# Performance work log

Measured on AMD Instinct MI355X. Metric: run time of the kernel, lower is better.

The kernel has to match this reference:

```python
import jax, jax.numpy as jnp
import numpy as np

EPS = 1e-6
INPUT_SIZE = 64
NUM_LEAVES = INPUT_SIZE
NUM_LAYERS = NUM_LEAVES - 1
BATCH = 262144
SINKHORN_ITERS = 20


def _clip01(v):
    return jnp.clip(v, EPS, 1.0 - EPS)


def _F_base(x, y, a, w0, w1):
    # Branches of F for a in [0.5, 2] (the non-recursive region), selected branchlessly.
    x = _clip01(x)
    y = _clip01(y)
    lin = w0 * x + w1 * y
    p = jnp.sqrt(3.0 / jnp.maximum(2.0 - a, EPS)) - 1.0
    g = (x ** (2.0 * w0) * y ** (2.0 * w1)) ** p
    rule0 = jnp.where((jnp.abs(x - 1.0) < EPS) & (jnp.abs(y - 1.0) < EPS), 1.0, 0.0)
    return jnp.where(
        jnp.abs(a - 2.0) < EPS, rule0,
        jnp.where(a >= 0.75, g,
                  jnp.where(a > 0.5, (3.0 - 4.0 * a) * lin + (4.0 * a - 2.0) * g, lin)))


def _F(x, y, a, w0, w1):
    # Full generalized_gcd F with the single-level De Morgan reflection for a < 0.5.
    x = _clip01(x)
    y = _clip01(y)
    hi = _F_base(x, y, a, w0, w1)
    a_ref = jnp.clip(1.0 - a, -1.0 + EPS, 2.0 - EPS)
    lo = 1.0 - _F_base(1.0 - x, 1.0 - y, a_ref, w0, w1)
    lin = w0 * x + w1 * y
    return jnp.where(jnp.abs(a - 0.5) < EPS, lin, jnp.where(a < 0.5, lo, hi))


def _sinkhorn(logits, n_iter=SINKHORN_ITERS):
    # Log-space Sinkhorn normalization -> (approximately) doubly-stochastic P.
    l = logits
    for _ in range(n_iter):
        l = l - jax.nn.logsumexp(l, axis=1, keepdims=True)
        l = l - jax.nn.logsumexp(l, axis=0, keepdims=True)
    return jnp.exp(l)


def setup_inputs() -> dict:
    key = jax.random.key(0)
    k1, k2, k3, k4 = jax.random.split(key, 4)
    x = jax.random.uniform(k1, (BATCH, INPUT_SIZE), dtype=jnp.float32)
    logits = jax.random.normal(k2, (INPUT_SIZE, NUM_LEAVES), dtype=jnp.float32)
    weights = jax.random.uniform(k3, (NUM_LAYERS,), dtype=jnp.float32)
    biases = jax.random.uniform(k4, (NUM_LAYERS,), dtype=jnp.float32)
    return {"x": x, "logits": logits, "weights": weights, "biases": biases}


def reference(x, logits, weights, biases):
    P = _sinkhorn(logits)                 # [INPUT_SIZE, NUM_LEAVES], columns sum to 1
    leaves = (x @ P).T                    # [NUM_LEAVES, BATCH]

    def step(carry, inp):
        leaf, w, b = inp
        nres = _F(carry, leaf, b, w, 1.0 - w)
        nres = jnp.where(jnp.isnan(nres), b, nres)  # NaN fallback to bias, as in torch forward
        return nres, None

    # Left-leaning tree: state_0 = leaf_0; state_i = F(state_{i-1}, leaf_i, b, w, 1-w)
    final, _ = jax.lax.scan(step, leaves[0], (leaves[1:], weights, biases))
    return final[:, None]                 # [BATCH, 1]
```

## Files before the change

kernel.cpp:

```cpp
#include <hip/hip_runtime.h>
#include <hip/hip_bf16.h>
#include <math.h>

#define EPS 1e-6f
#define N 64
#define NLAYERS 63
#define SINK_ITERS 20
#define LOG2E 1.4426950408889634f

typedef __attribute__((ext_vector_type(8))) short bf16x8;
typedef __attribute__((ext_vector_type(4))) float f32x4;

__device__ __forceinline__ float fast_log2(float v) {
#if __has_builtin(__builtin_amdgcn_logf)
  return __builtin_amdgcn_logf(v);
#else
  return log2f(v);
#endif
}
__device__ __forceinline__ float fast_exp2(float v) {
#if __has_builtin(__builtin_amdgcn_exp2f)
  return __builtin_amdgcn_exp2f(v);
#else
  return exp2f(v);
#endif
}

__device__ __forceinline__ unsigned short f2bf(float f) {
  unsigned int u = __float_as_uint(f);
  return (unsigned short)((u + 0x7FFFu + ((u >> 16) & 1u)) >> 16);
}

__device__ __forceinline__ bf16x8 pack8(float4 a, float4 b) {
  union { unsigned short us[8]; bf16x8 v; } u;
  u.us[0] = f2bf(a.x); u.us[1] = f2bf(a.y);
  u.us[2] = f2bf(a.z); u.us[3] = f2bf(a.w);
  u.us[4] = f2bf(b.x); u.us[5] = f2bf(b.y);
  u.us[6] = f2bf(b.z); u.us[7] = f2bf(b.w);
  return u.v;
}

__global__ __launch_bounds__(64) void sinkhorn_kernel(
    const float* __restrict__ logits,
    const float* __restrict__ weights,
    const float* __restrict__ biases,
    unsigned short* __restrict__ Pfrag,
    float* __restrict__ layers) {
  __shared__ float T[64 * 65 + 128];
  const int l = threadIdx.x;

  float K[64];
  {
    const float4* lr = (const float4*)(logits + (l << 6));
    #pragma unroll
    for (int q = 0; q < 16; ++q) {
      float4 t = lr[q];
      K[4*q+0] = fast_exp2(t.x * LOG2E);
      K[4*q+1] = fast_exp2(t.y * LOG2E);
      K[4*q+2] = fast_exp2(t.z * LOG2E);
      K[4*q+3] = fast_exp2(t.w * LOG2E);
    }
  }
  #pragma unroll
  for (int j = 0; j < 64; ++j) T[l * 65 + j] = K[j];
  __syncthreads();
  float KT[64];
  #pragma unroll
  for (int k = 0; k < 64; ++k) KT[k] = T[k * 65 + l];
  __syncthreads();

  float* Uv = &T[64 * 65];
  float* Vv = &T[64 * 65 + 64];
  const float4* Uv4 = (const float4*)Uv;
  const float4* Vv4 = (const float4*)Vv;
  Vv[l] = 1.0f;
  __syncthreads();

  float u = 1.0f;
  for (int it = 0; it < SINK_ITERS; ++it) {
    float s0 = 0.f, s1 = 0.f, s2 = 0.f, s3 = 0.f;
    #pragma unroll
    for (int q = 0; q < 16; ++q) {
      float4 v = Vv4[q];
      s0 = fmaf(K[4*q+0], v.x, s0);
      s1 = fmaf(K[4*q+1], v.y, s1);
      s2 = fmaf(K[4*q+2], v.z, s2);
      s3 = fmaf(K[4*q+3], v.w, s3);
    }
    u = 1.0f / ((s0 + s1) + (s2 + s3));
    __syncthreads();
    Uv[l] = u;
    __syncthreads();
    float c0 = 0.f, c1 = 0.f, c2 = 0.f, c3 = 0.f;
    #pragma unroll
    for (int q = 0; q < 16; ++q) {
      float4 uu = Uv4[q];
      c0 = fmaf(KT[4*q+0], uu.x, c0);
      c1 = fmaf(KT[4*q+1], uu.y, c1);
      c2 = fmaf(KT[4*q+2], uu.z, c2);
      c3 = fmaf(KT[4*q+3], uu.w, c3);
    }
    float v = 1.0f / ((c0 + c1) + (c2 + c3));
    __syncthreads();
    Vv[l] = v;
    __syncthreads();
  }

  #pragma unroll
  for (int j = 0; j < 64; ++j) T[l * 65 + j] = u * K[j] * Vv[j];
  __syncthreads();

  #pragma unroll
  for (int s = 0; s < 2; ++s)
    #pragma unroll
    for (int t = 0; t < 4; ++t) {
      union { unsigned short us[8]; bf16x8 v; } buf;
      #pragma unroll
      for (int j = 0; j < 8; ++j)
        buf.us[j] = f2bf(T[(s*32 + ((l >> 4) << 3) + j) * 65 + t*16 + (l & 15)]);
      *(bf16x8*)(Pfrag + (((s*4 + t) * 64 + l) << 3)) = buf.v;
    }

  if (l < NLAYERS) {
    float w0 = weights[l];
    float w1 = 1.0f - w0;
    float a  = biases[l];
    float e0, e1, cl, cg, sgn;
    if (fabsf(a - 0.5f) < EPS) {
      e0 = 0.f; e1 = 0.f; cl = 1.f; cg = 0.f; sgn = 1.f;
    } else {
      float ae;
      if (a < 0.5f) { sgn = -1.f; ae = fminf(fmaxf(1.0f - a, -1.0f + EPS), 2.0f - EPS); }
      else          { sgn =  1.f; ae = a; }
      float pp = sqrtf(3.0f / fmaxf(2.0f - ae, EPS)) - 1.0f;
      if (ae >= 0.75f) { cl = 0.0f;            cg = 1.0f; }
      else             { cl = 3.0f - 4.0f*ae;  cg = 4.0f*ae - 2.0f; }
      e0 = 2.0f * w0 * pp;
      e1 = 2.0f * w1 * pp;
    }
    float* Lr = layers + l * 8;
    Lr[0] = w0; Lr[1] = w1; Lr[2] = e0; Lr[3] = e1;
    Lr[4] = cl; Lr[5] = cg; Lr[6] = a;  Lr[7] = sgn;
  }
}

__global__ __launch_bounds__(256, 2) void scan_kernel(
    const float* __restrict__ x,
    const unsigned short* __restrict__ Pfrag,
    const float* __restrict__ layers,
    float* __restrict__ out) {
  __shared__ float Lv[256 * 36];
  const int tid = threadIdx.x;
  const int w = tid >> 6, l = tid & 63;
  const int q = l >> 4, c = l & 15;
  const size_t rowbase = (size_t)blockIdx.x << 8;
  const float4* Lp4 = (const float4*)layers;

  bf16x8 Bf[2][4];
  #pragma unroll
  for (int s = 0; s < 2; ++s)
    #pragma unroll
    for (int t = 0; t < 4; ++t)
      Bf[s][t] = *(const bf16x8*)(Pfrag + (((s*4 + t) * 64 + l) << 3));

  bf16x8 Af[4][2];
  #pragma unroll
  for (int i = 0; i < 4; ++i) {
    const float* rp = x + (rowbase + (w << 6) + (i << 4) + c) * 64 + (q << 3);
    float4 a0 = *(const float4*)(rp);
    float4 a1 = *(const float4*)(rp + 4);
    float4 b0 = *(const float4*)(rp + 32);
    float4 b1 = *(const float4*)(rp + 36);
    Af[i][0] = pack8(a0, a1);
    Af[i][1] = pack8(b0, b1);
  }

  float st = 0.f;
  #pragma unroll
  for (int half = 0; half < 2; ++half) {
    #pragma unroll
    for (int rt = 0; rt < 4; ++rt) {
      #pragma unroll
      for (int lt = 0; lt < 2; ++lt) {
        f32x4 acc = {0.f, 0.f, 0.f, 0.f};
        acc = __builtin_amdgcn_mfma_f32_16x16x32_bf16(Bf[0][(half<<1)+lt], Af[rt][0], acc, 0, 0, 0);
        acc = __builtin_amdgcn_mfma_f32_16x16x32_bf16(Bf[1][(half<<1)+lt], Af[rt][1], acc, 0, 0, 0);
        const int row  = (w << 6) + (rt << 4) + c;
        const int nloc = (lt << 4) + (q << 2);
        *(f32x4*)&Lv[row * 36 + nloc] = acc;
      }
    }
    f32x4 Lf[8];
    #pragma unroll
    for (int i = 0; i < 8; ++i)
      Lf[i] = *(f32x4*)&Lv[tid * 36 + (i << 2)];

    const int j0 = (half == 0) ? 1 : 32;
    const int nst = (half == 0) ? 31 : 32;

    float ylin[32], ylog[32];
    #pragma unroll
    for (int k = 0; k < 32; ++k) {
      if (k < nst) {
        const int j = j0 + k;
        const int jl = j - (half << 5);
        float4 p0 = Lp4[(j - 1) * 2];
        float4 p1 = Lp4[(j - 1) * 2 + 1];
        const float sgn = p1.w;
        const float off = fmaf(-0.5f, sgn, 0.5f);
        float yy = fminf(fmaxf(Lf[jl >> 2][jl & 3], EPS), 1.0f - EPS);
        float yr = fmaf(sgn, yy, off);
        ylin[k] = p0.y * yr;
        ylog[k] = p0.w * fast_log2(yr);
      }
    }

    if (half == 0) st = Lf[0][0];
    #pragma unroll
    for (int k = 0; k < 32; ++k) {
      if (k < nst) {
        const int j = j0 + k;
        float4 p0 = Lp4[(j - 1) * 2];
        float4 p1 = Lp4[(j - 1) * 2 + 1];
        const float sgn = p1.w;
        const float off = fmaf(-0.5f, sgn, 0.5f);
        float xx = fminf(fmaxf(st, EPS), 1.0f - EPS);
        xx = fmaf(sgn, xx, off);
        float lin = fmaf(p0.x, xx, ylin[k]);
        float g   = fast_exp2(fmaf(p0.z, fast_log2(xx), ylog[k]));
        float r   = fmaf(p1.x, lin, p1.y * g);
        st = fmaf(sgn, r, off);
      }
    }
  }

  out[rowbase + tid] = st;
}

extern "C" void kernel_launch(void* const* d_in, const int* in_sizes, int n_in,
                              void* d_out, int out_size, void* d_ws, size_t ws_size,
                              hipStream_t stream) {
  const float* x       = (const float*)d_in[0];
  const float* logits  = (const float*)d_in[1];
  const float* weights = (const float*)d_in[2];
  const float* biases  = (const float*)d_in[3];
  float* out = (float*)d_out;

  unsigned short* Pfrag = (unsigned short*)d_ws;
  float* layers = (float*)((char*)d_ws + 8 * 64 * 8 * sizeof(unsigned short));

  const int batch = out_size;

  hipLaunchKernelGGL(sinkhorn_kernel, dim3(1), dim3(64), 0, stream,
                     logits, weights, biases, Pfrag, layers);
  hipLaunchKernelGGL(scan_kernel, dim3(batch / 256), dim3(256), 0, stream,
                     x, Pfrag, layers, out);
}
```

Measured before the change: 120.5 us.

## Fold reflection signs and coefficients into layer table, chunk scan for occupancy

Precomputes per-layer combined reflection sign/offset, pre-multiplied linear weights and a log2 of the g coefficient, so each scan step uses fewer ops and the state stays in reflected space between layers. The scan is split into 8-layer chunks with a non-unrolled loop to cut register use, and launch bounds rise from 2 to 4 blocks per SM. The bf16 conversion now uses the packed hardware convert instruction, and x loads are issued before the fragment loads. Risks include changed rounding (hardware convert vs manual round-to-nearest-even), the -1e30 log-sentinel approach, and loop overhead from the non-unrolled chunks.

Result: no change. 119.8 us (-0.6%).

```diff
diff --git a/kernel.cpp b/kernel.cpp
--- a/kernel.cpp
+++ b/kernel.cpp
@@ -31,12 +31,17 @@
   return (unsigned short)((u + 0x7FFFu + ((u >> 16) & 1u)) >> 16);
 }
 
+__device__ __forceinline__ unsigned int cvt_pk_bf16(float lo, float hi) {
+  unsigned int r;
+  asm("v_cvt_pk_bf16_f32 %0, %1, %2" : "=v"(r) : "v"(lo), "v"(hi));
+  return r;
+}
 __device__ __forceinline__ bf16x8 pack8(float4 a, float4 b) {
-  union { unsigned short us[8]; bf16x8 v; } u;
-  u.us[0] = f2bf(a.x); u.us[1] = f2bf(a.y);
-  u.us[2] = f2bf(a.z); u.us[3] = f2bf(a.w);
-  u.us[4] = f2bf(b.x); u.us[5] = f2bf(b.y);
-  u.us[6] = f2bf(b.z); u.us[7] = f2bf(b.w);
+  union { unsigned int ui[4]; bf16x8 v; } u;
+  u.ui[0] = cvt_pk_bf16(a.x, a.y);
+  u.ui[1] = cvt_pk_bf16(a.z, a.w);
+  u.ui[2] = cvt_pk_bf16(b.x, b.y);
+  u.ui[3] = cvt_pk_bf16(b.z, b.w);
   return u.v;
 }
 
@@ -125,26 +130,92 @@
     float w0 = weights[l];
     float w1 = 1.0f - w0;
     float a  = biases[l];
-    float e0, e1, cl, cg, sgn;
+    float sgn, e0, e1, cw0, cw1, lcg;
     if (fabsf(a - 0.5f) < EPS) {
-      e0 = 0.f; e1 = 0.f; cl = 1.f; cg = 0.f; sgn = 1.f;
+      sgn = 1.f; e0 = 0.f; e1 = 0.f; cw0 = w0; cw1 = w1; lcg = -1.0e30f;
     } else {
       float ae;
       if (a < 0.5f) { sgn = -1.f; ae = fminf(fmaxf(1.0f - a, -1.0f + EPS), 2.0f - EPS); }
       else          { sgn =  1.f; ae = a; }
       float pp = sqrtf(3.0f / fmaxf(2.0f - ae, EPS)) - 1.0f;
+      float cl, cg;
       if (ae >= 0.75f) { cl = 0.0f;            cg = 1.0f; }
       else             { cl = 3.0f - 4.0f*ae;  cg = 4.0f*ae - 2.0f; }
-      e0 = 2.0f * w0 * pp;
-      e1 = 2.0f * w1 * pp;
-    }
+      e0  = 2.0f * w0 * pp;
+      e1  = 2.0f * w1 * pp;
+      cw0 = cl * w0;
+      cw1 = cl * w1;
+      lcg = (cg > 0.f) ? log2f(cg) : -1.0e30f;
+    }
+    float sgnp = 1.f;
+    if (l > 0) {
+      float ap = biases[l - 1];
+      sgnp = (fabsf(ap - 0.5f) < EPS) ? 1.f : (ap < 0.5f ? -1.f : 1.f);
+    }
+    float Sc = sgn * sgnp;
+    float Oc = 0.5f - 0.5f * Sc;
     float* Lr = layers + l * 8;
-    Lr[0] = w0; Lr[1] = w1; Lr[2] = e0; Lr[3] = e1;
-    Lr[4] = cl; Lr[5] = cg; Lr[6] = a;  Lr[7] = sgn;
-  }
-}
-
-__global__ __launch_bounds__(256, 2) void scan_kernel(
+    Lr[0] = sgn; Lr[1] = e1; Lr[2] = lcg; Lr[3] = cw1;
+    Lr[4] = Sc;  Lr[5] = Oc; Lr[6] = e0;  Lr[7] = cw0;
+  }
+}
+
+
+template<int HALF>
+__device__ __forceinline__ void do_gemm(const bf16x8 (&Bf)[2][4],
+                                        const bf16x8 (&Af)[4][2],
+                                        float* Lv, int w, int q, int c) {
+  #pragma unroll
+  for (int rt = 0; rt < 4; ++rt) {
+    #pragma unroll
+    for (int lt = 0; lt < 2; ++lt) {
+      f32x4 acc = {0.f, 0.f, 0.f, 0.f};
+      acc = __builtin_amdgcn_mfma_f32_16x16x32_bf16(Bf[0][(HALF << 1) + lt], Af[rt][0], acc, 0, 0, 0);
+      acc = __builtin_amdgcn_mfma_f32_16x16x32_bf16(Bf[1][(HALF << 1) + lt], Af[rt][1], acc, 0, 0, 0);
+      const int row  = (w << 6) + (rt << 4) + c;
+      const int nloc = (lt << 4) + (q << 2);
+      *(f32x4*)&Lv[row * 36 + nloc] = acc;
+    }
+  }
+}
+
+__device__ __forceinline__ void do_chunk(int L0, const float* Lrow,
+                                         const float4* Lp4, float& r) {
+  const int loc = L0 & 31;
+  f32x4 lf0 = *(const f32x4*)&Lrow[loc];
+  f32x4 lf1 = *(const f32x4*)&Lrow[loc + 4];
+  float lf[8] = {lf0[0], lf0[1], lf0[2], lf0[3], lf1[0], lf1[1], lf1[2], lf1[3]};
+
+  float ylin[8], ylg[8];
+  #pragma unroll
+  for (int k = 0; k < 8; ++k) {
+    if (L0 + k >= 1) {
+      float4 p0 = Lp4[(L0 + k - 1) * 2];
+      float off = fmaf(-0.5f, p0.x, 0.5f);
+      float yy  = fminf(fmaxf(lf[k], EPS), 1.0f - EPS);
+      float yr  = fmaf(p0.x, yy, off);
+      float ly  = fast_log2(yr);
+      ylg[k]  = fmaf(p0.y, ly, p0.z);
+      ylin[k] = p0.w * yr;
+    }
+  }
+
+  #pragma unroll
+  for (int k = 0; k < 8; ++k) {
+    if (L0 + k >= 1) {
+      float4 p1 = Lp4[(L0 + k - 1) * 2 + 1];
+      float cr = fminf(fmaxf(r, EPS), 1.0f - EPS);
+      float xr = fmaf(p1.x, cr, p1.y);
+      float lx = fast_log2(xr);
+      float g  = fast_exp2(fmaf(p1.z, lx, ylg[k]));
+      r = fmaf(p1.w, xr, ylin[k]) + g;
+    } else {
+      r = lf[0];
+    }
+  }
+}
+
+__global__ __launch_bounds__(256, 4) void scan_kernel(
     const float* __restrict__ x,
     const unsigned short* __restrict__ Pfrag,
     const float* __restrict__ layers,
@@ -156,6 +227,16 @@
   const size_t rowbase = (size_t)blockIdx.x << 8;
   const float4* Lp4 = (const float4*)layers;
 
+  float4 xa[4][4];
+  #pragma unroll
+  for (int i = 0; i < 4; ++i) {
+    const float* rp = x + (rowbase + (w << 6) + (i << 4) + c) * 64 + (q << 3);
+    xa[i][0] = *(const float4*)(rp);
+    xa[i][1] = *(const float4*)(rp + 4);
+    xa[i][2] = *(const float4*)(rp + 32);
+    xa[i][3] = *(const float4*)(rp + 36);
+  }
+
   bf16x8 Bf[2][4];
   #pragma unroll
   for (int s = 0; s < 2; ++s)
@@ -166,75 +247,25 @@
   bf16x8 Af[4][2];
   #pragma unroll
   for (int i = 0; i < 4; ++i) {
-    const float* rp = x + (rowbase + (w << 6) + (i << 4) + c) * 64 + (q << 3);
-    float4 a0 = *(const float4*)(rp);
-    float4 a1 = *(const float4*)(rp + 4);
-    float4 b0 = *(const float4*)(rp + 32);
-    float4 b1 = *(const float4*)(rp + 36);
-    Af[i][0] = pack8(a0, a1);
-    Af[i][1] = pack8(b0, b1);
-  }
-
-  float st = 0.f;
-  #pragma unroll
-  for (int half = 0; half < 2; ++half) {
-    #pragma unroll
-    for (int rt = 0; rt < 4; ++rt) {
-      #pragma unroll
-      for (int lt = 0; lt < 2; ++lt) {
-        f32x4 acc = {0.f, 0.f, 0.f, 0.f};
-        acc = __builtin_amdgcn_mfma_f32_16x16x32_bf16(Bf[0][(half<<1)+lt], Af[rt][0], acc, 0, 0, 0);
-        acc = __builtin_amdgcn_mfma_f32_16x16x32_bf16(Bf[1][(half<<1)+lt], Af[rt][1], acc, 0, 0, 0);
-        const int row  = (w << 6) + (rt << 4) + c;
-        const int nloc = (lt << 4) + (q << 2);
-        *(f32x4*)&Lv[row * 36 + nloc] = acc;
-      }
-    }
-    f32x4 Lf[8];
-    #pragma unroll
-    for (int i = 0; i < 8; ++i)
-      Lf[i] = *(f32x4*)&Lv[tid * 36 + (i << 2)];
-
-    const int j0 = (half == 0) ? 1 : 32;
-    const int nst = (half == 0) ? 31 : 32;
-
-    float ylin[32], ylog[32];
-    #pragma unroll
-    for (int k = 0; k < 32; ++k) {
-      if (k < nst) {
-        const int j = j0 + k;
-        const int jl = j - (half << 5);
-        float4 p0 = Lp4[(j - 1) * 2];
-        float4 p1 = Lp4[(j - 1) * 2 + 1];
-        const float sgn = p1.w;
-        const float off = fmaf(-0.5f, sgn, 0.5f);
-        float yy = fminf(fmaxf(Lf[jl >> 2][jl & 3], EPS), 1.0f - EPS);
-        float yr = fmaf(sgn, yy, off);
-        ylin[k] = p0.y * yr;
-        ylog[k] = p0.w * fast_log2(yr);
-      }
-    }
-
-    if (half == 0) st = Lf[0][0];
-    #pragma unroll
-    for (int k = 0; k < 32; ++k) {
-      if (k < nst) {
-        const int j = j0 + k;
-        float4 p0 = Lp4[(j - 1) * 2];
-        float4 p1 = Lp4[(j - 1) * 2 + 1];
-        const float sgn = p1.w;
-        const float off = fmaf(-0.5f, sgn, 0.5f);
-        float xx = fminf(fmaxf(st, EPS), 1.0f - EPS);
-        xx = fmaf(sgn, xx, off);
-        float lin = fmaf(p0.x, xx, ylin[k]);
-        float g   = fast_exp2(fmaf(p0.z, fast_log2(xx), ylog[k]));
-        float r   = fmaf(p1.x, lin, p1.y * g);
-        st = fmaf(sgn, r, off);
-      }
-    }
-  }
-
-  out[rowbase + tid] = st;
+    Af[i][0] = pack8(xa[i][0], xa[i][1]);
+    Af[i][1] = pack8(xa[i][2], xa[i][3]);
+  }
+
+  float r = 0.f;
+  const float* Lrow = &Lv[tid * 36];
+
+  do_gemm<0>(Bf, Af, Lv, w, q, c);
+  #pragma unroll 1
+  for (int cch = 0; cch < 4; ++cch)
+    do_chunk(cch * 8, Lrow, Lp4, r);
+
+  do_gemm<1>(Bf, Af, Lv, w, q, c);
+  #pragma unroll 1
+  for (int cch = 0; cch < 4; ++cch)
+    do_chunk(32 + cch * 8, Lrow, Lp4, r);
+
+  const float sgnL = layers[62 * 8];
+  out[rowbase + tid] = fmaf(sgnL, r, fmaf(-0.5f, sgnL, 0.5f));
 }
 
 extern "C" void kernel_launch(void* const* d_in, const int* in_sizes, int n_in,
```
